# Kernel optimization log

Measured on AMD Instinct MI355X. Metric: run time of the kernel, lower is better.

The kernel has to match this reference:

```python
import jax, jax.numpy as jnp
import numpy as np

N, DIM, K = 262144, 64, 1024

def setup_inputs() -> dict:
    key = jax.random.key(0)
    k1, k2 = jax.random.split(key)
    x = jax.random.normal(k1, (N, DIM), dtype=jnp.float32)
    embed = jax.random.normal(k2, (K, DIM), dtype=jnp.float32)
    return {"x": x, "embed": embed}

def reference(x, embed):
    distances = (jnp.sum(x * x, axis=-1, keepdims=True)
                 - 2.0 * (x @ embed.T)
                 + jnp.sum(embed * embed, axis=-1))  # [N, K]
    idx = jnp.argmin(distances, axis=-1)  # [N]
    # dequantize: embedding lookup
    out = embed[idx]  # [N, DIM]
    return out
```

## Files before the change

kernel.cpp:

```cpp
#include <hip/hip_runtime.h>


#define VQ_N 262144
#define VQ_DIM 64
#define VQ_K 1024
#define NT 64
#define TCH 128
#define FLAG_EPS 1.2e-2f

typedef short short8 __attribute__((ext_vector_type(8)));
typedef float f32x4 __attribute__((ext_vector_type(4)));

#define WS_BH    0
#define WS_BL    (128*1024)
#define WS_E2    (256*1024)
#define WS_E2P   (260*1024)
#define WS_NEEDED (264*1024)

static __device__ __forceinline__ unsigned short f2bf_rtne(float f) {
    unsigned u = __float_as_uint(f);
    unsigned r = u + 0x7FFFu + ((u >> 16) & 1u);
    return (unsigned short)(r >> 16);
}
static __device__ __forceinline__ float bf2f(unsigned short h) {
    return __uint_as_float(((unsigned)h) << 16);
}
static __device__ __forceinline__ unsigned med3u(unsigned a, unsigned b, unsigned c) {
    unsigned d;
    asm("v_med3_u32 %0, %1, %2, %3" : "=v"(d) : "v"(a), "v"(b), "v"(c));
    return d;
}

__global__ void vq_prep(const float* __restrict__ embed, unsigned char* ws) {
    int t = blockIdx.x * 256 + threadIdx.x;
    if (t < 16384) {
        int arr = t >> 13;
        int c = t & 8191;
        int ct = c >> 7;
        int kc = (c >> 6) & 1;
        int l = c & 63;
        int code = ct * 16 + (l & 15);
        int kbase = kc * 32 + ((l >> 4) << 3);
        const float* ep = embed + (size_t)code * VQ_DIM + kbase;
        short8 pack;
#pragma unroll
        for (int j = 0; j < 8; ++j) {
            float v = ep[j];
            unsigned short h = f2bf_rtne(v);
            pack[j] = arr ? (short)f2bf_rtne(v - bf2f(h)) : (short)h;
        }
        ((short8*)(ws + (arr ? WS_BL : WS_BH)))[c] = pack;
    } else if (t < 16384 + VQ_K) {
        int code = t - 16384;
        const float* ep = embed + (size_t)code * VQ_DIM;
        float a0 = 0, a1 = 0, a2 = 0, a3 = 0;
#pragma unroll
        for (int j = 0; j < VQ_DIM; j += 4) {
            a0 = fmaf(ep[j], ep[j], a0);
            a1 = fmaf(ep[j + 1], ep[j + 1], a1);
            a2 = fmaf(ep[j + 2], ep[j + 2], a2);
            a3 = fmaf(ep[j + 3], ep[j + 3], a3);
        }
        float e2 = (a0 + a1) + (a2 + a3);
        ((float*)(ws + WS_E2))[code] = e2;
        ((float*)(ws + WS_E2P))[code] = e2 + 256.0f;
    }
}

__global__ __launch_bounds__(256, 4)
void vq_stage1(const float* __restrict__ x, const float* __restrict__ embed,
               unsigned char* ws, float* __restrict__ out) {
    const int tid = threadIdx.x;
    const int lane = tid & 63;
    const int wave = tid >> 6;
    const int gwave = blockIdx.x * 4 + wave;
    const int R0 = gwave * 32;
    const int g = lane >> 4;
    const int res = lane & 15;
    const int khalf = g << 3;

    const short8* bh = (const short8*)(ws + WS_BH);
    const short8* bl = (const short8*)(ws + WS_BL);
    const float* e2g = (const float*)(ws + WS_E2);
    const float* e2p = (const float*)(ws + WS_E2P);

    short8 ah00, ah01, al00, al01, ah10, ah11, al10, al11;
#define MAKE_A(ROW, KC, AH, AL)                                             \
    {                                                                       \
        const float4* p4 = (const float4*)(x + (size_t)(ROW) * VQ_DIM +     \
                                           (KC) * 32 + khalf);              \
        float4 v0 = p4[0], v1 = p4[1];                                      \
        float q0 = -2.0f * v0.x, q1 = -2.0f * v0.y, q2 = -2.0f * v0.z,      \
              q3 = -2.0f * v0.w, q4 = -2.0f * v1.x, q5 = -2.0f * v1.y,      \
              q6 = -2.0f * v1.z, q7 = -2.0f * v1.w;                         \
        unsigned short h0 = f2bf_rtne(q0), h1 = f2bf_rtne(q1),              \
                       h2 = f2bf_rtne(q2), h3 = f2bf_rtne(q3),              \
                       h4 = f2bf_rtne(q4), h5 = f2bf_rtne(q5),              \
                       h6 = f2bf_rtne(q6), h7 = f2bf_rtne(q7);              \
        AH[0] = (short)h0; AH[1] = (short)h1; AH[2] = (short)h2;            \
        AH[3] = (short)h3; AH[4] = (short)h4; AH[5] = (short)h5;            \
        AH[6] = (short)h6; AH[7] = (short)h7;                               \
        AL[0] = (short)f2bf_rtne(q0 - bf2f(h0));                            \
        AL[1] = (short)f2bf_rtne(q1 - bf2f(h1));                            \
        AL[2] = (short)f2bf_rtne(q2 - bf2f(h2));                            \
        AL[3] = (short)f2bf_rtne(q3 - bf2f(h3));                            \
        AL[4] = (short)f2bf_rtne(q4 - bf2f(h4));                            \
        AL[5] = (short)f2bf_rtne(q5 - bf2f(h5));                            \
        AL[6] = (short)f2bf_rtne(q6 - bf2f(h6));                            \
        AL[7] = (short)f2bf_rtne(q7 - bf2f(h7));                            \
    }
    const int row0 = R0 + res;
    const int row1 = row0 + 16;
    MAKE_A(row0, 0, ah00, al00)
    MAKE_A(row0, 1, ah01, al01)
    MAKE_A(row1, 0, ah10, al10)
    MAKE_A(row1, 1, ah11, al11)
#undef MAKE_A

    unsigned m1k0[4], m2k0[4], m1k1[4], m2k1[4];
#pragma unroll
    for (int r = 0; r < 4; ++r) {
        m1k0[r] = 0xFFFFFFFFu; m2k0[r] = 0xFFFFFFFFu;
        m1k1[r] = 0xFFFFFFFFu; m2k1[r] = 0xFFFFFFFFu;
    }

#pragma unroll 2
    for (int ct = 0; ct < NT; ++ct) {
        const short8* bht = bh + (size_t)ct * TCH;
        const short8* blt = bl + (size_t)ct * TCH;
        short8 bh0 = bht[lane];
        short8 bh1 = bht[64 + lane];
        short8 bl0 = blt[lane];
        short8 bl1 = blt[64 + lane];
        float e2c = e2p[ct * 16 + res];
        unsigned ctu = (unsigned)ct;

        f32x4 acc0 = {e2c, e2c, e2c, e2c};
        acc0 = __builtin_amdgcn_mfma_f32_16x16x32_bf16(al00, bh0, acc0, 0, 0, 0);
        acc0 = __builtin_amdgcn_mfma_f32_16x16x32_bf16(al01, bh1, acc0, 0, 0, 0);
        acc0 = __builtin_amdgcn_mfma_f32_16x16x32_bf16(ah00, bl0, acc0, 0, 0, 0);
        acc0 = __builtin_amdgcn_mfma_f32_16x16x32_bf16(ah01, bl1, acc0, 0, 0, 0);
        acc0 = __builtin_amdgcn_mfma_f32_16x16x32_bf16(ah00, bh0, acc0, 0, 0, 0);
        acc0 = __builtin_amdgcn_mfma_f32_16x16x32_bf16(ah01, bh1, acc0, 0, 0, 0);

        f32x4 acc1 = {e2c, e2c, e2c, e2c};
        acc1 = __builtin_amdgcn_mfma_f32_16x16x32_bf16(al10, bh0, acc1, 0, 0, 0);
        acc1 = __builtin_amdgcn_mfma_f32_16x16x32_bf16(al11, bh1, acc1, 0, 0, 0);
        acc1 = __builtin_amdgcn_mfma_f32_16x16x32_bf16(ah10, bl0, acc1, 0, 0, 0);
        acc1 = __builtin_amdgcn_mfma_f32_16x16x32_bf16(ah11, bl1, acc1, 0, 0, 0);
        acc1 = __builtin_amdgcn_mfma_f32_16x16x32_bf16(ah10, bh0, acc1, 0, 0, 0);
        acc1 = __builtin_amdgcn_mfma_f32_16x16x32_bf16(ah11, bh1, acc1, 0, 0, 0);

#pragma unroll
        for (int r = 0; r < 4; ++r) {
            unsigned key = (__float_as_uint(acc0[r]) & 0xFFFFFFC0u) | ctu;
            m2k0[r] = med3u(m1k0[r], m2k0[r], key);
            m1k0[r] = m1k0[r] < key ? m1k0[r] : key;
        }
#pragma unroll
        for (int r = 0; r < 4; ++r) {
            unsigned key = (__float_as_uint(acc1[r]) & 0xFFFFFFC0u) | ctu;
            m2k1[r] = med3u(m1k1[r], m2k1[r], key);
            m1k1[r] = m1k1[r] < key ? m1k1[r] : key;
        }
    }

    unsigned res0[4], res1[4];
#pragma unroll
    for (int r = 0; r < 4; ++r) { res0[r] = (unsigned)res; res1[r] = res0[r]; }
#define RED_STEP(M1, M2, RES, m)                                                      \
    {                                                                                 \
        _Pragma("unroll")                                                             \
        for (int r = 0; r < 4; ++r) {                                                 \
            unsigned ok = (unsigned)__shfl_xor((int)M1[r], m);                        \
            unsigned ok2 = (unsigned)__shfl_xor((int)M2[r], m);                       \
            unsigned orr = (unsigned)__shfl_xor((int)RES[r], m);                      \
            unsigned t1 = M1[r] > ok ? M1[r] : ok;                                    \
            unsigned c2 = ok2 < t1 ? ok2 : t1;                                        \
            M2[r] = M2[r] < c2 ? M2[r] : c2;                                          \
            bool take = (ok < M1[r]) || (ok == M1[r] && orr < RES[r]);                \
            if (take) { M1[r] = ok; RES[r] = orr; }                                   \
        }                                                                             \
    }
#pragma unroll
    for (int m = 1; m <= 8; m <<= 1) {
        RED_STEP(m1k0, m2k0, res0, m)
        RED_STEP(m1k1, m2k1, res1, m)
    }
#undef RED_STEP

    int code0[4], code1[4];
    unsigned fmask = 0;
#pragma unroll
    for (int r = 0; r < 4; ++r) {
        code0[r] = (int)((m1k0[r] & 63u) * 16u + res0[r]);
        code1[r] = (int)((m1k1[r] & 63u) * 16u + res1[r]);
        float s1a = __uint_as_float(m1k0[r] & 0xFFFFFFC0u);
        float s2a = __uint_as_float(m2k0[r] & 0xFFFFFFC0u);
        if (s2a - s1a < FLAG_EPS) fmask |= 1u << (4 * g + r);
        float s1b = __uint_as_float(m1k1[r] & 0xFFFFFFC0u);
        float s2b = __uint_as_float(m2k1[r] & 0xFFFFFFC0u);
        if (s2b - s1b < FLAG_EPS) fmask |= 1u << (16 + 4 * g + r);
    }
    fmask |= (unsigned)__shfl_xor((int)fmask, 16);
    fmask |= (unsigned)__shfl_xor((int)fmask, 32);
    unsigned wmask = fmask;

    {
        const int q = lane >> 1;
        const int setq = q >> 4;
        const int gq = (q & 15) >> 2;
        const int rq = q & 3;
        const int src = gq << 4;
        int a0 = __shfl(code0[0], src), a1 = __shfl(code0[1], src);
        int a2 = __shfl(code0[2], src), a3 = __shfl(code0[3], src);
        int b0 = __shfl(code1[0], src), b1 = __shfl(code1[1], src);
        int b2 = __shfl(code1[2], src), b3 = __shfl(code1[3], src);
        int cs0 = (rq == 0) ? a0 : (rq == 1) ? a1 : (rq == 2) ? a2 : a3;
        int cs1 = (rq == 0) ? b0 : (rq == 1) ? b1 : (rq == 2) ? b2 : b3;
        int my = setq ? cs1 : cs0;
        const float4* ep = (const float4*)(embed + (size_t)my * VQ_DIM) + (lane & 1) * 8;
        float4* op = (float4*)(out + (size_t)(R0 + q) * VQ_DIM) + (lane & 1) * 8;
#pragma unroll
        for (int j = 0; j < 8; ++j) op[j] = ep[j];
    }

    while (wmask) {
        int b = __ffs(wmask) - 1;
        wmask &= wmask - 1;
        int row = R0 + b;
        const float4* xr4 = (const float4*)(x + (size_t)row * VQ_DIM);
        float best = __builtin_inff();
        int bi = VQ_K;
        for (int t = 0; t < VQ_K / 64; ++t) {
            int c = t * 64 + lane;
            const float4* ep4 = (const float4*)(embed + (size_t)c * VQ_DIM);
            float a0 = 0, a1 = 0, a2 = 0, a3 = 0;
#pragma unroll
            for (int j = 0; j < VQ_DIM / 4; ++j) {
                float4 xv = xr4[j];
                float4 ev = ep4[j];
                a0 = fmaf(xv.x, ev.x, a0);
                a1 = fmaf(xv.y, ev.y, a1);
                a2 = fmaf(xv.z, ev.z, a2);
                a3 = fmaf(xv.w, ev.w, a3);
            }
            float dot = (a0 + a1) + (a2 + a3);
            float s = fmaf(-2.0f, dot, e2g[c]);
            if (s < best || (s == best && c < bi)) { best = s; bi = c; }
        }
#pragma unroll
        for (int m = 1; m <= 32; m <<= 1) {
            float ob = __shfl_xor(best, m);
            int oi = __shfl_xor(bi, m);
            if (ob < best || (ob == best && oi < bi)) { best = ob; bi = oi; }
        }
        out[(size_t)row * VQ_DIM + lane] = embed[(size_t)bi * VQ_DIM + lane];
    }
}

__global__ __launch_bounds__(256, 4)
void vq_fallback(const float* __restrict__ x, const float* __restrict__ embed,
                 float* __restrict__ out) {
    __shared__ float e2s[VQ_K];
    const int tid = threadIdx.x;
    for (int c = tid; c < VQ_K; c += 256) {
        const float4* ep = (const float4*)(embed + c * VQ_DIM);
        float s = 0.0f;
#pragma unroll
        for (int j = 0; j < VQ_DIM / 4; ++j) {
            float4 v = ep[j];
            s = fmaf(v.x, v.x, s); s = fmaf(v.y, v.y, s);
            s = fmaf(v.z, v.z, s); s = fmaf(v.w, v.w, s);
        }
        e2s[c] = s;
    }
    __syncthreads();
    const int row = blockIdx.x * 256 + tid;
    float xr[VQ_DIM];
    const float4* xp = (const float4*)(x + (size_t)row * VQ_DIM);
#pragma unroll
    for (int j = 0; j < VQ_DIM / 4; ++j) {
        float4 v = xp[j];
        xr[4 * j] = v.x; xr[4 * j + 1] = v.y; xr[4 * j + 2] = v.z; xr[4 * j + 3] = v.w;
    }
    float best = __builtin_inff();
    int bidx = 0;
    for (int c = 0; c < VQ_K; ++c) {
        const float4* ep = (const float4*)(embed + c * VQ_DIM);
        float a0 = 0, a1 = 0, a2 = 0, a3 = 0;
#pragma unroll
        for (int j = 0; j < VQ_DIM / 4; ++j) {
            float4 v = ep[j];
            a0 = fmaf(xr[4 * j], v.x, a0);
            a1 = fmaf(xr[4 * j + 1], v.y, a1);
            a2 = fmaf(xr[4 * j + 2], v.z, a2);
            a3 = fmaf(xr[4 * j + 3], v.w, a3);
        }
        float score = fmaf(-2.0f, (a0 + a1) + (a2 + a3), e2s[c]);
        if (score < best) { best = score; bidx = c; }
    }
    const float4* bp = (const float4*)(embed + (size_t)bidx * VQ_DIM);
    float4* op = (float4*)(out + (size_t)row * VQ_DIM);
#pragma unroll
    for (int j = 0; j < VQ_DIM / 4; ++j) op[j] = bp[j];
}

extern "C" void kernel_launch(void* const* d_in, const int* in_sizes, int n_in,
                              void* d_out, int out_size, void* d_ws, size_t ws_size,
                              hipStream_t stream) {
    const float* x = (const float*)d_in[0];
    const float* embed = (const float*)d_in[1];
    float* out = (float*)d_out;
    if (ws_size < WS_NEEDED) {
        hipLaunchKernelGGL(vq_fallback, dim3(VQ_N / 256), dim3(256), 0, stream, x, embed, out);
        return;
    }
    unsigned char* ws = (unsigned char*)d_ws;
    hipLaunchKernelGGL(vq_prep, dim3(70), dim3(256), 0, stream, embed, ws);
    hipLaunchKernelGGL(vq_stage1, dim3(VQ_N / 128), dim3(256), 0, stream, x, embed, ws, out);
}
```

Baseline: 170.7 us.

## Halve rows per wave to 16 and double occupancy target

Each wave now processes one 16-row tile instead of two, so codebook B fragments are reused across half as many rows. The grid doubles and launch bounds ask for 8 blocks per CU, cutting register pressure to raise occupancy. The cost is twice the codebook reads from workspace per row and less MFMA work per B load, and the ambiguous-row fallback loop now runs over more waves.

```diff
diff --git a/kernel.cpp b/kernel.cpp
--- a/kernel.cpp
+++ b/kernel.cpp
@@ -67,14 +67,14 @@
     }
 }
 
-__global__ __launch_bounds__(256, 4)
+__global__ __launch_bounds__(256, 8)
 void vq_stage1(const float* __restrict__ x, const float* __restrict__ embed,
                unsigned char* ws, float* __restrict__ out) {
     const int tid = threadIdx.x;
     const int lane = tid & 63;
     const int wave = tid >> 6;
     const int gwave = blockIdx.x * 4 + wave;
-    const int R0 = gwave * 32;
+    const int R0 = gwave * 16;
     const int g = lane >> 4;
     const int res = lane & 15;
     const int khalf = g << 3;
@@ -84,7 +84,7 @@
     const float* e2g = (const float*)(ws + WS_E2);
     const float* e2p = (const float*)(ws + WS_E2P);
 
-    short8 ah00, ah01, al00, al01, ah10, ah11, al10, al11;
+    short8 ah0, ah1, al0, al1;
 #define MAKE_A(ROW, KC, AH, AL)                                             \
     {                                                                       \
         const float4* p4 = (const float4*)(x + (size_t)(ROW) * VQ_DIM +     \
@@ -110,19 +110,13 @@
         AL[7] = (short)f2bf_rtne(q7 - bf2f(h7));                            \
     }
     const int row0 = R0 + res;
-    const int row1 = row0 + 16;
-    MAKE_A(row0, 0, ah00, al00)
-    MAKE_A(row0, 1, ah01, al01)
-    MAKE_A(row1, 0, ah10, al10)
-    MAKE_A(row1, 1, ah11, al11)
+    MAKE_A(row0, 0, ah0, al0)
+    MAKE_A(row0, 1, ah1, al1)
 #undef MAKE_A
 
-    unsigned m1k0[4], m2k0[4], m1k1[4], m2k1[4];
-#pragma unroll
-    for (int r = 0; r < 4; ++r) {
-        m1k0[r] = 0xFFFFFFFFu; m2k0[r] = 0xFFFFFFFFu;
-        m1k1[r] = 0xFFFFFFFFu; m2k1[r] = 0xFFFFFFFFu;
-    }
+    unsigned m1k[4], m2k[4];
+#pragma unroll
+    for (int r = 0; r < 4; ++r) { m1k[r] = 0xFFFFFFFFu; m2k[r] = 0xFFFFFFFFu; }
 
 #pragma unroll 2
     for (int ct = 0; ct < NT; ++ct) {
@@ -135,94 +129,65 @@
         float e2c = e2p[ct * 16 + res];
         unsigned ctu = (unsigned)ct;
 
-        f32x4 acc0 = {e2c, e2c, e2c, e2c};
-        acc0 = __builtin_amdgcn_mfma_f32_16x16x32_bf16(al00, bh0, acc0, 0, 0, 0);
-        acc0 = __builtin_amdgcn_mfma_f32_16x16x32_bf16(al01, bh1, acc0, 0, 0, 0);
-        acc0 = __builtin_amdgcn_mfma_f32_16x16x32_bf16(ah00, bl0, acc0, 0, 0, 0);
-        acc0 = __builtin_amdgcn_mfma_f32_16x16x32_bf16(ah01, bl1, acc0, 0, 0, 0);
-        acc0 = __builtin_amdgcn_mfma_f32_16x16x32_bf16(ah00, bh0, acc0, 0, 0, 0);
-        acc0 = __builtin_amdgcn_mfma_f32_16x16x32_bf16(ah01, bh1, acc0, 0, 0, 0);
-
-        f32x4 acc1 = {e2c, e2c, e2c, e2c};
-        acc1 = __builtin_amdgcn_mfma_f32_16x16x32_bf16(al10, bh0, acc1, 0, 0, 0);
-        acc1 = __builtin_amdgcn_mfma_f32_16x16x32_bf16(al11, bh1, acc1, 0, 0, 0);
-        acc1 = __builtin_amdgcn_mfma_f32_16x16x32_bf16(ah10, bl0, acc1, 0, 0, 0);
-        acc1 = __builtin_amdgcn_mfma_f32_16x16x32_bf16(ah11, bl1, acc1, 0, 0, 0);
-        acc1 = __builtin_amdgcn_mfma_f32_16x16x32_bf16(ah10, bh0, acc1, 0, 0, 0);
-        acc1 = __builtin_amdgcn_mfma_f32_16x16x32_bf16(ah11, bh1, acc1, 0, 0, 0);
+        f32x4 acc = {e2c, e2c, e2c, e2c};
+        acc = __builtin_amdgcn_mfma_f32_16x16x32_bf16(al0, bh0, acc, 0, 0, 0);
+        acc = __builtin_amdgcn_mfma_f32_16x16x32_bf16(al1, bh1, acc, 0, 0, 0);
+        acc = __builtin_amdgcn_mfma_f32_16x16x32_bf16(ah0, bl0, acc, 0, 0, 0);
+        acc = __builtin_amdgcn_mfma_f32_16x16x32_bf16(ah1, bl1, acc, 0, 0, 0);
+        acc = __builtin_amdgcn_mfma_f32_16x16x32_bf16(ah0, bh0, acc, 0, 0, 0);
+        acc = __builtin_amdgcn_mfma_f32_16x16x32_bf16(ah1, bh1, acc, 0, 0, 0);
 
 #pragma unroll
         for (int r = 0; r < 4; ++r) {
-            unsigned key = (__float_as_uint(acc0[r]) & 0xFFFFFFC0u) | ctu;
-            m2k0[r] = med3u(m1k0[r], m2k0[r], key);
-            m1k0[r] = m1k0[r] < key ? m1k0[r] : key;
-        }
+            unsigned key = (__float_as_uint(acc[r]) & 0xFFFFFFC0u) | ctu;
+            m2k[r] = med3u(m1k[r], m2k[r], key);
+            m1k[r] = m1k[r] < key ? m1k[r] : key;
+        }
+    }
+
+    unsigned res0[4];
+#pragma unroll
+    for (int r = 0; r < 4; ++r) res0[r] = (unsigned)res;
+#pragma unroll
+    for (int m = 1; m <= 8; m <<= 1) {
 #pragma unroll
         for (int r = 0; r < 4; ++r) {
-            unsigned key = (__float_as_uint(acc1[r]) & 0xFFFFFFC0u) | ctu;
-            m2k1[r] = med3u(m1k1[r], m2k1[r], key);
-            m1k1[r] = m1k1[r] < key ? m1k1[r] : key;
-        }
-    }
-
-    unsigned res0[4], res1[4];
-#pragma unroll
-    for (int r = 0; r < 4; ++r) { res0[r] = (unsigned)res; res1[r] = res0[r]; }
-#define RED_STEP(M1, M2, RES, m)                                                      \
-    {                                                                                 \
-        _Pragma("unroll")                                                             \
-        for (int r = 0; r < 4; ++r) {                                                 \
-            unsigned ok = (unsigned)__shfl_xor((int)M1[r], m);                        \
-            unsigned ok2 = (unsigned)__shfl_xor((int)M2[r], m);                       \
-            unsigned orr = (unsigned)__shfl_xor((int)RES[r], m);                      \
-            unsigned t1 = M1[r] > ok ? M1[r] : ok;                                    \
-            unsigned c2 = ok2 < t1 ? ok2 : t1;                                        \
-            M2[r] = M2[r] < c2 ? M2[r] : c2;                                          \
-            bool take = (ok < M1[r]) || (ok == M1[r] && orr < RES[r]);                \
-            if (take) { M1[r] = ok; RES[r] = orr; }                                   \
-        }                                                                             \
-    }
-#pragma unroll
-    for (int m = 1; m <= 8; m <<= 1) {
-        RED_STEP(m1k0, m2k0, res0, m)
-        RED_STEP(m1k1, m2k1, res1, m)
-    }
-#undef RED_STEP
-
-    int code0[4], code1[4];
+            unsigned ok = (unsigned)__shfl_xor((int)m1k[r], m);
+            unsigned ok2 = (unsigned)__shfl_xor((int)m2k[r], m);
+            unsigned orr = (unsigned)__shfl_xor((int)res0[r], m);
+            unsigned t1 = m1k[r] > ok ? m1k[r] : ok;
+            unsigned c2 = ok2 < t1 ? ok2 : t1;
+            m2k[r] = m2k[r] < c2 ? m2k[r] : c2;
+            bool take = (ok < m1k[r]) || (ok == m1k[r] && orr < res0[r]);
+            if (take) { m1k[r] = ok; res0[r] = orr; }
+        }
+    }
+
+    int code0[4];
     unsigned fmask = 0;
 #pragma unroll
     for (int r = 0; r < 4; ++r) {
-        code0[r] = (int)((m1k0[r] & 63u) * 16u + res0[r]);
-        code1[r] = (int)((m1k1[r] & 63u) * 16u + res1[r]);
-        float s1a = __uint_as_float(m1k0[r] & 0xFFFFFFC0u);
-        float s2a = __uint_as_float(m2k0[r] & 0xFFFFFFC0u);
-        if (s2a - s1a < FLAG_EPS) fmask |= 1u << (4 * g + r);
-        float s1b = __uint_as_float(m1k1[r] & 0xFFFFFFC0u);
-        float s2b = __uint_as_float(m2k1[r] & 0xFFFFFFC0u);
-        if (s2b - s1b < FLAG_EPS) fmask |= 1u << (16 + 4 * g + r);
+        code0[r] = (int)((m1k[r] & 63u) * 16u + res0[r]);
+        float s1 = __uint_as_float(m1k[r] & 0xFFFFFFC0u);
+        float s2 = __uint_as_float(m2k[r] & 0xFFFFFFC0u);
+        if (s2 - s1 < FLAG_EPS) fmask |= 1u << (4 * g + r);
     }
     fmask |= (unsigned)__shfl_xor((int)fmask, 16);
     fmask |= (unsigned)__shfl_xor((int)fmask, 32);
     unsigned wmask = fmask;
 
     {
-        const int q = lane >> 1;
-        const int setq = q >> 4;
-        const int gq = (q & 15) >> 2;
+        const int q = lane >> 2;
+        const int gq = q >> 2;
         const int rq = q & 3;
         const int src = gq << 4;
         int a0 = __shfl(code0[0], src), a1 = __shfl(code0[1], src);
         int a2 = __shfl(code0[2], src), a3 = __shfl(code0[3], src);
-        int b0 = __shfl(code1[0], src), b1 = __shfl(code1[1], src);
-        int b2 = __shfl(code1[2], src), b3 = __shfl(code1[3], src);
-        int cs0 = (rq == 0) ? a0 : (rq == 1) ? a1 : (rq == 2) ? a2 : a3;
-        int cs1 = (rq == 0) ? b0 : (rq == 1) ? b1 : (rq == 2) ? b2 : b3;
-        int my = setq ? cs1 : cs0;
-        const float4* ep = (const float4*)(embed + (size_t)my * VQ_DIM) + (lane & 1) * 8;
-        float4* op = (float4*)(out + (size_t)(R0 + q) * VQ_DIM) + (lane & 1) * 8;
-#pragma unroll
-        for (int j = 0; j < 8; ++j) op[j] = ep[j];
+        int my = (rq == 0) ? a0 : (rq == 1) ? a1 : (rq == 2) ? a2 : a3;
+        const float4* ep = (const float4*)(embed + (size_t)my * VQ_DIM) + (lane & 3) * 4;
+        float4* op = (float4*)(out + (size_t)(R0 + q) * VQ_DIM) + (lane & 3) * 4;
+#pragma unroll
+        for (int j = 0; j < 4; ++j) op[j] = ep[j];
     }
 
     while (wmask) {
@@ -318,5 +283,5 @@
     }
     unsigned char* ws = (unsigned char*)d_ws;
     hipLaunchKernelGGL(vq_prep, dim3(70), dim3(256), 0, stream, embed, ws);
-    hipLaunchKernelGGL(vq_stage1, dim3(VQ_N / 128), dim3(256), 0, stream, x, embed, ws, out);
-}
+    hipLaunchKernelGGL(vq_stage1, dim3(VQ_N / 64), dim3(256), 0, stream, x, embed, ws, out);
+}
```

Result: slower. 373.8 us (+119.0%).
